# Kernel optimization log

Hardware: AMD Instinct MI355X
Metric: run time of the kernel (lower is better)

The kernel has to match this reference:

```python
import jax, jax.numpy as jnp
import numpy as np

N = 2708       # hardcoded in the original forward (Cora)
INS = 1433
OUTS = 64
M = 8          # N_mechs
HID = 64       # conditioner hidden width
LEAK = 0.2
NEG = -1e9


def setup_inputs() -> dict:
    key = jax.random.key(0)
    ks = jax.random.split(key, 9)
    x = jax.random.normal(ks[0], (N, INS), dtype=jnp.float32)
    adj = jax.random.randint(ks[1], (N, N), 0, 2) > 0  # bool mask
    adj = adj | jnp.eye(N, dtype=bool)                 # ensure self-loops so softmax is well-defined
    s = 1.0 / np.sqrt(INS)
    W = jax.random.normal(ks[2], (M, INS, OUTS), dtype=jnp.float32) * s
    a_src = jax.random.normal(ks[3], (M, OUTS), dtype=jnp.float32) * (1.0 / np.sqrt(OUTS))
    a_dst = jax.random.normal(ks[4], (M, OUTS), dtype=jnp.float32) * (1.0 / np.sqrt(OUTS))
    Wc1 = jax.random.normal(ks[5], (INS, HID), dtype=jnp.float32) * s
    bc1 = jnp.zeros((HID,), dtype=jnp.float32)
    Wc2 = jax.random.normal(ks[6], (HID, 2 * M), dtype=jnp.float32) * (1.0 / np.sqrt(HID))
    bc2 = jnp.zeros((2 * M,), dtype=jnp.float32)
    return {"x": x, "adj": adj, "W": W, "a_src": a_src, "a_dst": a_dst,
            "Wc1": Wc1, "bc1": bc1, "Wc2": Wc2, "bc2": bc2}


def reference(x, adj, W, a_src, a_dst, Wc1, bc1, Wc2, bc2):
    # dropout is identity in eval mode.
    # Conditioner MLP applied per node (vectorized over the Python loop in the original):
    cond = jax.nn.relu(x @ Wc1 + bc1) @ Wc2 + bc2          # [N, 2M]
    c = cond.reshape(N, 2, M)                               # matches cond.view(2708, 2, -1)
    gamma = c[:, 0, :].T                                    # [M, N] per-node scalar gamma per mechanism
    beta = c[:, 1, :].T                                     # [M, N]
    # All mechanisms batched: project + FiLM modulate
    h = jnp.einsum('nf,mfo->mno', x, W)                     # [M, N, OUTS]
    h = gamma[:, :, None] * h + beta[:, :, None]
    # GAT scoring: e_ij = LeakyReLU(a_src.h_i + a_dst.h_j), masked by adj
    e_src = jnp.einsum('mno,mo->mn', h, a_src)              # [M, N]
    e_dst = jnp.einsum('mno,mo->mn', h, a_dst)              # [M, N]
    e = jax.nn.leaky_relu(e_src[:, :, None] + e_dst[:, None, :], LEAK)  # [M, N, N]
    e = jnp.where(adj[None, :, :], e, NEG)
    attn = jax.nn.softmax(e, axis=-1)                       # [M, N, N]
    out = jnp.einsum('mnk,mko->mno', attn, h)               # [M, N, OUTS]
    # concat=True: cat over mechanisms along feature dim
    out = jnp.transpose(out, (1, 0, 2)).reshape(N, M * OUTS)  # [N, M*OUTS]
    return out
```

## Files before the change

### kernel.cpp

```cpp
#include <hip/hip_runtime.h>

#define NN   2708
#define INS  1433
#define MM   8
#define NP   2720
#define WPR  85
#define KP   1440
#define NKC  45
#define RP   2752
#define C9   576
#define OC   512

#define CAN_ASRC 0
#define CAN_ADST 512
#define CAN_BC1  1024
#define CAN_BC2  1088
#define CAN_WC2  1104
#define CAN_TOT  2128

#define ADJ_WAVES (NN * 11)
#define ADJBLK ((ADJ_WAVES + 3) / 4)
#define XBLK   1935
#define WTBLK  (9 * 23)
#define PACK_TOT (ADJBLK + XBLK + WTBLK + 1)

typedef unsigned short u16;
typedef unsigned int   u32;
typedef __attribute__((ext_vector_type(8))) short bf16x8;
typedef __attribute__((ext_vector_type(4))) float f32x4;

static __device__ __forceinline__ u16 f2bfu(float f) {
    union { float f; u32 u; } v; v.f = f;
    u32 u = v.u;
    u32 r = (u + 0x7fffu + ((u >> 16) & 1u)) >> 16;
    return (u16)r;
}
static __device__ __forceinline__ float bfu2f(u16 b) {
    union { u32 u; float f; } v; v.u = ((u32)b) << 16;
    return v.f;
}

static __device__ __forceinline__ int xfp32_of(const int* ctr) {
    int s = 0;
    #pragma unroll
    for (int k = 0; k < 32; ++k) s += ctr[k];
    return s > 32;
}
static __device__ __forceinline__ int aflag_decode(int b) {
    if (b & 2)  return 3;
    if (b & 4)  return 4;
    if (b & 8)  return 5;
    if (b & 1)  return 1;
    if (b & 16) return 0;
    return 2;
}

__global__ void k_probe(const u32* __restrict__ x_raw, const u32* __restrict__ adj_raw,
                        int* __restrict__ ctr) {
    const int b = blockIdx.x, t = threadIdx.x;
    __shared__ int sred[4];
    if (b < 32) {
        int local = 0;
        #pragma unroll
        for (int k = 0; k < 8; ++k) {
            u32 v = x_raw[b * 2048 + k * 256 + t];
            u32 lo = v & 0xffffu, hi = v >> 16;
            if ((lo & 0x7f80u) == 0u && lo != 0u) local++;
            if ((hi & 0x7f80u) == 0u && hi != 0u) local++;
        }
        #pragma unroll
        for (int off = 32; off > 0; off >>= 1) local += __shfl_xor(local, off, 64);
        if ((t & 63) == 0) sred[t >> 6] = local;
        __syncthreads();
        if (t == 0) ctr[b] = sred[0] + sred[1] + sred[2] + sred[3];
    } else {
        int fl = 0;
        #pragma unroll
        for (int k = 0; k < 8; ++k) {
            int w = (b - 32) * 2048 + k * 256 + t;
            u32 v = adj_raw[w];
            if (v > 1u)           fl |= 1;
            if (v == 0x3f803f80u) fl |= 2;
            if (v == 0x3f800000u) fl |= 4;
            if (v == 0x3c003c00u) fl |= 8;
            if ((w & 1) && v)     fl |= 16;
        }
        #pragma unroll
        for (int off = 32; off > 0; off >>= 1) fl |= __shfl_xor(fl, off, 64);
        if ((t & 63) == 0) sred[t >> 6] = fl;
        __syncthreads();
        if (t == 0) ctr[b] = sred[0] | sred[1] | sred[2] | sred[3];
    }
}

static __device__ __forceinline__ u16 load_as_bf16(const void* p, size_t idx, int fp32) {
    if (fp32) return f2bfu(((const float*)p)[idx]);
    return ((const u16*)p)[idx];
}
static __device__ __forceinline__ float load_as_f32(const void* p, size_t idx, int fp32) {
    if (fp32) return ((const float*)p)[idx];
    return bfu2f(((const u16*)p)[idx]);
}

__global__ void k_pack(const void* __restrict__ x, const void* __restrict__ adj,
                       const void* __restrict__ W, const void* __restrict__ Wc1,
                       const void* a_src, const void* a_dst, const void* bc1,
                       const void* bc2, const void* Wc2,
                       u16* __restrict__ xpf, u16* __restrict__ WTf,
                       u32* __restrict__ adjT, float* __restrict__ canon,
                       const int* __restrict__ ctr) {
    __shared__ float lds[64][65];
    __shared__ int sflags[2];
    const int t = threadIdx.x;
    if (t < 64) {
        int v = ctr[t];
        int cnt  = (t < 32) ? v : 0;
        int bits = (t >= 32) ? v : 0;
        #pragma unroll
        for (int off = 32; off > 0; off >>= 1) {
            cnt  += __shfl_xor(cnt, off, 64);
            bits |= __shfl_xor(bits, off, 64);
        }
        if (t == 0) { sflags[0] = cnt; sflags[1] = bits; }
    }
    __syncthreads();
    const int fp32 = sflags[0] > 32;

    const int bid = blockIdx.x;
    if (bid < ADJBLK) {
        const int f = aflag_decode(sflags[1]);
        const int wid  = bid * 4 + (t >> 6);
        const int lane = t & 63;
        const int i = wid / 11;
        const int c256 = wid - i * 11;
        if (i >= NN) return;
        const int jb0 = c256 * 256;
        #pragma unroll
        for (int s = 0; s < 4; ++s) {
            const int jb = jb0 + s * 64;
            if (jb >= NP) break;
            const int j = jb + lane;
            int v = 0;
            if (j < NN) {
                size_t idx = (size_t)i * NN + j;
                if      (f == 0) v = ((const int*)adj)[idx] != 0;
                else if (f == 1) v = ((const unsigned char*)adj)[idx] != 0;
                else if (f == 2) v = ((const long long*)adj)[idx] != 0;
                else if (f == 4) v = ((const float*)adj)[idx] != 0.f;
                else             v = ((const u16*)adj)[idx] != 0;
            }
            unsigned long long mask = __ballot(v);
            if (lane == 0) {
                const int ww = jb >> 5;
                adjT[(size_t)ww * NP + i] = (u32)mask;
                if (ww + 1 < WPR) adjT[(size_t)(ww + 1) * NP + i] = (u32)(mask >> 32);
            }
        }
    } else if (bid < ADJBLK + XBLK) {
        const int base = (bid - ADJBLK) * 2048 + t;
        #pragma unroll
        for (int s = 0; s < 8; ++s) {
            const int e = base + s * 256;
            const int t1 = e >> 9, sub = e & 511;
            const int r = sub >> 5, kloc = sub & 31;
            const int it = t1 / NKC, kc = t1 - it * NKC;
            const int row = it * 16 + r, col = kc * 32 + kloc;
            u16 v = 0;
            if (row < NN && col < INS) v = load_as_bf16(x, (size_t)row * INS + col, fp32);
            xpf[e] = v;
        }
    } else if (bid < ADJBLK + XBLK + WTBLK) {
        const int b2 = bid - ADJBLK - XBLK;
        const int mblk = b2 / 23, ktile = b2 - mblk * 23;
        #pragma unroll
        for (int ii = 0; ii < 16; ++ii) {
            int l = t * 16 + ii;
            int k_in = l >> 6, o = l & 63;
            int k = ktile * 64 + k_in;
            float v = 0.f;
            if (k < INS) {
                if (mblk < 8) v = load_as_f32(W, ((size_t)mblk * INS + k) * 64 + o, fp32);
                else          v = load_as_f32(Wc1, (size_t)k * 64 + o, fp32);
            }
            lds[k_in][o] = v;
        }
        __syncthreads();
        #pragma unroll
        for (int ii = 0; ii < 16; ++ii) {
            int e2 = t * 16 + ii;
            int ct2 = e2 >> 10, kc2 = (e2 >> 9) & 1;
            int r = (e2 >> 5) & 15, kloc = e2 & 31;
            int kc = ktile * 2 + kc2;
            if (kc < NKC) {
                int ct = mblk * 4 + ct2;
                WTf[(((size_t)ct * NKC + kc) * 16 + r) * 32 + kloc] =
                    f2bfu(lds[kc2 * 32 + kloc][ct2 * 16 + r]);
            }
        }
    } else {
        for (int e = t; e < CAN_TOT; e += 256) {
            float v;
            if      (e < CAN_ADST) v = load_as_f32(a_src, e - CAN_ASRC, fp32);
            else if (e < CAN_BC1)  v = load_as_f32(a_dst, e - CAN_ADST, fp32);
            else if (e < CAN_BC2)  v = load_as_f32(bc1,  e - CAN_BC1, fp32);
            else if (e < CAN_WC2)  v = load_as_f32(bc2,  e - CAN_BC2, fp32);
            else                   v = load_as_f32(Wc2,  e - CAN_WC2, fp32);
            canon[e] = v;
        }
    }
}

__launch_bounds__(64)
__global__ void k_gemm(const u16* __restrict__ xpf, const u16* __restrict__ WTf,
                       float* __restrict__ h_pre) {
    const int lane = threadIdx.x;
    const int r    = lane & 15;
    const int quad = lane >> 4;
    const int it0  = blockIdx.x * 2;
    const int ct0  = blockIdx.y * 2;

    const u16* aP0 = xpf + (size_t)it0 * NKC * 512 + r * 32 + quad * 8;
    const u16* aP1 = aP0 + (size_t)NKC * 512;
    const u16* bP0 = WTf + (size_t)ct0 * NKC * 512 + r * 32 + quad * 8;
    const u16* bP1 = bP0 + (size_t)NKC * 512;

    f32x4 acc[2][2];
    #pragma unroll
    for (int a = 0; a < 2; ++a)
        #pragma unroll
        for (int b = 0; b < 2; ++b) acc[a][b] = (f32x4){0.f, 0.f, 0.f, 0.f};

    #pragma unroll 3
    for (int kc = 0; kc < NKC; ++kc) {
        bf16x8 a0 = *(const bf16x8*)(aP0 + kc * 512);
        bf16x8 a1 = *(const bf16x8*)(aP1 + kc * 512);
        bf16x8 b0 = *(const bf16x8*)(bP0 + kc * 512);
        bf16x8 b1 = *(const bf16x8*)(bP1 + kc * 512);
        acc[0][0] = __builtin_amdgcn_mfma_f32_16x16x32_bf16(a0, b0, acc[0][0], 0, 0, 0);
        acc[0][1] = __builtin_amdgcn_mfma_f32_16x16x32_bf16(a0, b1, acc[0][1], 0, 0, 0);
        acc[1][0] = __builtin_amdgcn_mfma_f32_16x16x32_bf16(a1, b0, acc[1][0], 0, 0, 0);
        acc[1][1] = __builtin_amdgcn_mfma_f32_16x16x32_bf16(a1, b1, acc[1][1], 0, 0, 0);
    }

    #pragma unroll
    for (int a = 0; a < 2; ++a) {
        #pragma unroll
        for (int reg = 0; reg < 4; ++reg) {
            const int ii = (it0 + a) * 16 + quad * 4 + reg;
            if (ii < NN) {
                float* orow = h_pre + (size_t)ii * C9 + ct0 * 16;
                orow[ 0 + r] = acc[a][0][reg];
                orow[16 + r] = acc[a][1][reg];
            }
        }
    }
}

__launch_bounds__(256)
__global__ void k_film(const float* __restrict__ h_pre, const float* __restrict__ canon,
                       u16* __restrict__ HTf, float* __restrict__ e_srcP,
                       float* __restrict__ e_dstP) {
    const int m  = blockIdx.y;
    const int n0 = blockIdx.x * 32;
    const int t  = threadIdx.x, wave = t >> 6, o = t & 63;
    __shared__ u16 hbuf[32][66];

    const float wg = canon[CAN_WC2 + o * 16 + m];
    const float wb = canon[CAN_WC2 + o * 16 + m + 8];
    const float as = canon[CAN_ASRC + m * 64 + o];
    const float ad = canon[CAN_ADST + m * 64 + o];
    const float b1 = canon[CAN_BC1 + o];
    const float g0 = canon[CAN_BC2 + m], b0 = canon[CAN_BC2 + m + 8];

    #pragma unroll
    for (int it = 0; it < 8; ++it) {
        const int nl = wave * 8 + it, n = n0 + nl;
        const bool valid = n < NN;
        float hv = 0.f;
        if (valid) hv = h_pre[(size_t)n * C9 + 512 + o] + b1;
        hv = hv > 0.f ? hv : 0.f;
        float pg = hv * wg, pb = hv * wb;
        #pragma unroll
        for (int off = 32; off > 0; off >>= 1) {
            pg += __shfl_xor(pg, off, 64);
            pb += __shfl_xor(pb, off, 64);
        }
        const float g = pg + g0, bb = pb + b0;
        float h = 0.f;
        if (valid) h = g * h_pre[(size_t)n * C9 + m * 64 + o] + bb;
        float ps = h * as, pd = h * ad;
        #pragma unroll
        for (int off = 32; off > 0; off >>= 1) {
            ps += __shfl_xor(ps, off, 64);
            pd += __shfl_xor(pd, off, 64);
        }
        if (o == 0) { e_srcP[m * NP + n] = ps; e_dstP[m * NP + n] = pd; }
        hbuf[nl][o] = f2bfu(h);
    }
    __syncthreads();
    u32* ht32 = (u32*)(HTf + ((size_t)m * WPR + (n0 >> 5)) * 2048);
    #pragma unroll
    for (int rep = 0; rep < 4; ++rep) {
        const int idx = rep * 256 + t;
        const int oo = idx >> 4, jp = idx & 15;
        ht32[idx] = (u32)hbuf[2 * jp][oo] | ((u32)hbuf[2 * jp + 1][oo] << 16);
    }
}

__global__ void k_prep(const float* __restrict__ e_srcP, const float* __restrict__ e_dstP,
                       float* __restrict__ E1P, float* __restrict__ E2P,
                       float* __restrict__ F1P, float* __restrict__ F2P) {
    const int m = blockIdx.x, sl = blockIdx.y, t = threadIdx.x;
    const float* ed = e_dstP + m * NP;
    const float* es = e_srcP + m * NP;
    float mx = -3.0e38f;
    for (int j = t; j < NP; j += 256) mx = fmaxf(mx, ed[j]);
    #pragma unroll
    for (int off = 32; off > 0; off >>= 1) mx = fmaxf(mx, __shfl_xor(mx, off, 64));
    __shared__ float sm[4];
    if ((t & 63) == 0) sm[t >> 6] = mx;
    __syncthreads();
    const float maxd = fmaxf(fmaxf(sm[0], sm[1]), fmaxf(sm[2], sm[3]));
    const int j0 = sl * (NP / 8);
    for (int j = j0 + t; j < j0 + NP / 8; j += 256) {
        const float d = ed[j] - maxd;
        E1P[m * NP + j] = __expf(d);
        E2P[m * NP + j] = __expf(0.2f * d);
    }
    for (int i = j0 + t; i < j0 + NP / 8; i += 256) {
        const float v = es[i] + maxd;
        const float rmax = v > 0.f ? v : 0.2f * v;
        F1P[m * NP + i] = __expf(v - rmax);
        F2P[m * NP + i] = __expf(0.2f * v - rmax);
    }
}

__launch_bounds__(256)
__global__ void k_attn(const u32* __restrict__ adjT, const float* __restrict__ F1P,
                       const float* __restrict__ F2P, const float* __restrict__ E1P,
                       const float* __restrict__ E2P, const u16* __restrict__ HTf,
                       void* __restrict__ outv, const int* __restrict__ ctr) {
    const int m = blockIdx.y, i0 = blockIdx.x * 16;
    const int t = threadIdx.x;
    const int wave = t >> 6, lane = t & 63;
    const int r = lane & 15, quad = lane >> 4;
    const int i = min(i0 + r, NN - 1);

    __shared__ float sE[2 * NP];
    __shared__ u32 sAdj[WPR * 16];

    for (int idx = t; idx < NP; idx += 256) {
        sE[idx]      = E1P[m * NP + idx];
        sE[NP + idx] = E2P[m * NP + idx];
    }
    for (int w = t; w < WPR * 16; w += 256) {
        const int tile = w >> 4, rr = w & 15;
        sAdj[w] = adjT[(size_t)tile * NP + min(i0 + rr, NN - 1)];
    }
    __syncthreads();

    const float F1 = F1P[m * NP + i], F2 = F2P[m * NP + i];
    const u16* hbase = HTf + (size_t)m * WPR * 2048 + r * 32 + quad * 8;

    f32x4 acc[4], accl;
    #pragma unroll
    for (int nt = 0; nt < 4; ++nt) acc[nt] = (f32x4){0.f, 0.f, 0.f, 0.f};
    accl = (f32x4){0.f, 0.f, 0.f, 0.f};

    bf16x8 ones;
    #pragma unroll
    for (int kk = 0; kk < 8; ++kk) ones[kk] = (short)0x3f80;

    #pragma unroll 2
    for (int jc = wave * 32; jc < NP; jc += 128) {
        const int jb = jc + quad * 8;
        const int tile = jc >> 5;
        const float4 a0 = *(const float4*)(sE + jb);
        const float4 a1 = *(const float4*)(sE + jb + 4);
        const float4 b0 = *(const float4*)(sE + NP + jb);
        const float4 b1 = *(const float4*)(sE + NP + jb + 4);
        const u32 w = sAdj[tile * 16 + r];
        const u32 mask8 = (w >> (quad * 8)) & 0xffu;
        float p[8];
        p[0] = fmaxf(F1 * a0.x, F2 * b0.x);
        p[1] = fmaxf(F1 * a0.y, F2 * b0.y);
        p[2] = fmaxf(F1 * a0.z, F2 * b0.z);
        p[3] = fmaxf(F1 * a0.w, F2 * b0.w);
        p[4] = fmaxf(F1 * a1.x, F2 * b1.x);
        p[5] = fmaxf(F1 * a1.y, F2 * b1.y);
        p[6] = fmaxf(F1 * a1.z, F2 * b1.z);
        p[7] = fmaxf(F1 * a1.w, F2 * b1.w);
        bf16x8 af;
        #pragma unroll
        for (int kk = 0; kk < 8; ++kk) {
            const float pv = ((mask8 >> kk) & 1u) ? p[kk] : 0.f;
            af[kk] = (short)f2bfu(pv);
        }
        const u16* ht = hbase + (size_t)tile * 2048;
        #pragma unroll
        for (int nt = 0; nt < 4; ++nt) {
            bf16x8 bf = *(const bf16x8*)(ht + nt * 512);
            acc[nt] = __builtin_amdgcn_mfma_f32_16x16x32_bf16(af, bf, acc[nt], 0, 0, 0);
        }
        accl = __builtin_amdgcn_mfma_f32_16x16x32_bf16(af, ones, accl, 0, 0, 0);
    }

    __syncthreads();
    float* red = sE;
    #pragma unroll
    for (int nt = 0; nt < 4; ++nt)
        #pragma unroll
        for (int reg = 0; reg < 4; ++reg)
            red[(wave * 64 + lane) * 21 + nt * 4 + reg] = acc[nt][reg];
    #pragma unroll
    for (int reg = 0; reg < 4; ++reg)
        red[(wave * 64 + lane) * 21 + 16 + reg] = accl[reg];
    __syncthreads();
    if (wave != 0) return;

    #pragma unroll
    for (int nt = 0; nt < 4; ++nt)
        #pragma unroll
        for (int reg = 0; reg < 4; ++reg)
            acc[nt][reg] = red[lane * 21 + nt * 4 + reg] + red[(64 + lane) * 21 + nt * 4 + reg]
                         + red[(128 + lane) * 21 + nt * 4 + reg] + red[(192 + lane) * 21 + nt * 4 + reg];
    #pragma unroll
    for (int reg = 0; reg < 4; ++reg)
        accl[reg] = red[lane * 21 + 16 + reg] + red[(64 + lane) * 21 + 16 + reg]
                  + red[(128 + lane) * 21 + 16 + reg] + red[(192 + lane) * 21 + 16 + reg];

    const int ofp32 = xfp32_of(ctr);
    #pragma unroll
    for (int reg = 0; reg < 4; ++reg) {
        const int ii = i0 + quad * 4 + reg;
        if (ii < NN) {
            const float lr = accl[reg];
            const float inv = (lr > 0.f) ? 1.f / lr : 0.f;
            #pragma unroll
            for (int nt = 0; nt < 4; ++nt) {
                const float o = acc[nt][reg] * inv;
                const size_t idx = (size_t)ii * OC + m * 64 + nt * 16 + r;
                if (ofp32) ((float*)outv)[idx] = o;
                else       ((u16*)outv)[idx]   = f2bfu(o);
            }
        }
    }
}

extern "C" void kernel_launch(void* const* d_in, const int* in_sizes, int n_in,
                              void* d_out, int out_size, void* d_ws, size_t ws_size,
                              hipStream_t stream) {
    (void)in_sizes; (void)n_in; (void)out_size; (void)ws_size;
    const void* x     = d_in[0];
    const void* adj   = d_in[1];
    const void* W     = d_in[2];
    const void* a_src = d_in[3];
    const void* a_dst = d_in[4];
    const void* Wc1   = d_in[5];
    const void* bc1   = d_in[6];
    const void* Wc2   = d_in[7];
    const void* bc2   = d_in[8];

    char* ws = (char*)d_ws;
    size_t off = 0;
    auto alloc = [&](size_t bytes) -> void* {
        void* p = ws + off;
        off += (bytes + 255) & ~(size_t)255;
        return p;
    };
    u16*   xpf     = (u16*)  alloc((size_t)RP * KP * 2);
    u16*   WTf     = (u16*)  alloc((size_t)C9 * KP * 2);
    float* h_pre   = (float*)alloc((size_t)NN * C9 * 4);
    float* e_srcP  = (float*)alloc((size_t)MM * NP * 4);
    float* e_dstP  = (float*)alloc((size_t)MM * NP * 4);
    float* E1P     = (float*)alloc((size_t)MM * NP * 4);
    float* E2P     = (float*)alloc((size_t)MM * NP * 4);
    float* F1P     = (float*)alloc((size_t)MM * NP * 4);
    float* F2P     = (float*)alloc((size_t)MM * NP * 4);
    u16*   HTf     = (u16*)  alloc((size_t)MM * WPR * 2048 * 2);
    u32*   adjT    = (u32*)  alloc((size_t)WPR * NP * 4);
    float* canon   = (float*)alloc((size_t)CAN_TOT * 4);
    int*   ctr     = (int*)  alloc(256);

    hipLaunchKernelGGL(k_probe, dim3(64), dim3(256), 0, stream,
                       (const u32*)x, (const u32*)adj, ctr);
    hipLaunchKernelGGL(k_pack, dim3(PACK_TOT), dim3(256), 0, stream,
                       x, adj, W, Wc1, a_src, a_dst, bc1, bc2, Wc2,
                       xpf, WTf, adjT, canon, ctr);
    hipLaunchKernelGGL(k_gemm, dim3(RP / 32, 18), dim3(64), 0, stream, xpf, WTf, h_pre);
    hipLaunchKernelGGL(k_film, dim3(NP / 32, MM), dim3(256), 0, stream,
                       h_pre, canon, HTf, e_srcP, e_dstP);
    hipLaunchKernelGGL(k_prep, dim3(MM, 8), dim3(256), 0, stream,
                       e_srcP, e_dstP, E1P, E2P, F1P, F2P);
    hipLaunchKernelGGL(k_attn, dim3((NN + 15) / 16, MM), dim3(256), 0, stream,
                       adjT, F1P, F2P, E1P, E2P, HTf, d_out, ctr);
}
```

Measured before the change: 196.9 us.

## Fuse softmax prep into film and attention kernels via atomic max

Removes the separate k_prep kernel. The per-mechanism e_dst max is now computed in k_film with an order-preserving uint atomicMax. The exp factors are recomputed inside k_attn while it stages to LDS. bf16 packing switches to packed hardware conversion intrinsics, and the output dtype flag is computed once per block into shared memory. This saves a launch and intermediate global arrays, at the cost of redundant exp work in every attention block. It also relies on atomic initialization in k_pack, and padded rows beyond NN in k_film may feed zero values into the max.

```diff
diff --git a/kernel.cpp b/kernel.cpp
--- a/kernel.cpp
+++ b/kernel.cpp
@@ -1,4 +1,5 @@
 #include <hip/hip_runtime.h>
+#include <hip/hip_bf16.h>
 
 #define NN   2708
 #define INS  1433
@@ -39,13 +40,20 @@
     union { u32 u; float f; } v; v.u = ((u32)b) << 16;
     return v.f;
 }
-
-static __device__ __forceinline__ int xfp32_of(const int* ctr) {
-    int s = 0;
-    #pragma unroll
-    for (int k = 0; k < 32; ++k) s += ctr[k];
-    return s > 32;
-}
+static __device__ __forceinline__ u32 pk_bf16(float a, float b) {
+    union { __hip_bfloat162 h; u32 w; } p;
+    p.h = __float22bfloat162_rn(make_float2(a, b));
+    return p.w;
+}
+static __device__ __forceinline__ u32 fkey(float f) {
+    u32 u = __float_as_uint(f);
+    return (u & 0x80000000u) ? ~u : (u | 0x80000000u);
+}
+static __device__ __forceinline__ float funkey(u32 k) {
+    u32 u = (k & 0x80000000u) ? (k & 0x7fffffffu) : ~k;
+    return __uint_as_float(u);
+}
+
 static __device__ __forceinline__ int aflag_decode(int b) {
     if (b & 2)  return 3;
     if (b & 4)  return 4;
@@ -108,7 +116,7 @@
                        const void* bc2, const void* Wc2,
                        u16* __restrict__ xpf, u16* __restrict__ WTf,
                        u32* __restrict__ adjT, float* __restrict__ canon,
-                       const int* __restrict__ ctr) {
+                       u32* __restrict__ maxdKey, const int* __restrict__ ctr) {
     __shared__ float lds[64][65];
     __shared__ int sflags[2];
     const int t = threadIdx.x;
@@ -198,6 +206,7 @@
             }
         }
     } else {
+        if (t < 8) maxdKey[t] = 0u;
         for (int e = t; e < CAN_TOT; e += 256) {
             float v;
             if      (e < CAN_ADST) v = load_as_f32(a_src, e - CAN_ASRC, fp32);
@@ -259,11 +268,12 @@
 __launch_bounds__(256)
 __global__ void k_film(const float* __restrict__ h_pre, const float* __restrict__ canon,
                        u16* __restrict__ HTf, float* __restrict__ e_srcP,
-                       float* __restrict__ e_dstP) {
+                       float* __restrict__ e_dstP, u32* __restrict__ maxdKey) {
     const int m  = blockIdx.y;
     const int n0 = blockIdx.x * 32;
     const int t  = threadIdx.x, wave = t >> 6, o = t & 63;
-    __shared__ u16 hbuf[32][66];
+    __shared__ float hbuf[32][66];
+    __shared__ float smx[4];
 
     const float wg = canon[CAN_WC2 + o * 16 + m];
     const float wb = canon[CAN_WC2 + o * 16 + m + 8];
@@ -272,6 +282,7 @@
     const float b1 = canon[CAN_BC1 + o];
     const float g0 = canon[CAN_BC2 + m], b0 = canon[CAN_BC2 + m + 8];
 
+    float mxd = -3.0e38f;
     #pragma unroll
     for (int it = 0; it < 8; ++it) {
         const int nl = wave * 8 + it, n = n0 + nl;
@@ -295,51 +306,29 @@
             pd += __shfl_xor(pd, off, 64);
         }
         if (o == 0) { e_srcP[m * NP + n] = ps; e_dstP[m * NP + n] = pd; }
-        hbuf[nl][o] = f2bfu(h);
-    }
+        mxd = fmaxf(mxd, pd);
+        hbuf[nl][o] = h;
+    }
+    if (o == 0) smx[wave] = mxd;
     __syncthreads();
+    if (t == 0) {
+        const float bm = fmaxf(fmaxf(smx[0], smx[1]), fmaxf(smx[2], smx[3]));
+        atomicMax(&maxdKey[m], fkey(bm));
+    }
     u32* ht32 = (u32*)(HTf + ((size_t)m * WPR + (n0 >> 5)) * 2048);
     #pragma unroll
     for (int rep = 0; rep < 4; ++rep) {
         const int idx = rep * 256 + t;
         const int oo = idx >> 4, jp = idx & 15;
-        ht32[idx] = (u32)hbuf[2 * jp][oo] | ((u32)hbuf[2 * jp + 1][oo] << 16);
-    }
-}
-
-__global__ void k_prep(const float* __restrict__ e_srcP, const float* __restrict__ e_dstP,
-                       float* __restrict__ E1P, float* __restrict__ E2P,
-                       float* __restrict__ F1P, float* __restrict__ F2P) {
-    const int m = blockIdx.x, sl = blockIdx.y, t = threadIdx.x;
-    const float* ed = e_dstP + m * NP;
-    const float* es = e_srcP + m * NP;
-    float mx = -3.0e38f;
-    for (int j = t; j < NP; j += 256) mx = fmaxf(mx, ed[j]);
-    #pragma unroll
-    for (int off = 32; off > 0; off >>= 1) mx = fmaxf(mx, __shfl_xor(mx, off, 64));
-    __shared__ float sm[4];
-    if ((t & 63) == 0) sm[t >> 6] = mx;
-    __syncthreads();
-    const float maxd = fmaxf(fmaxf(sm[0], sm[1]), fmaxf(sm[2], sm[3]));
-    const int j0 = sl * (NP / 8);
-    for (int j = j0 + t; j < j0 + NP / 8; j += 256) {
-        const float d = ed[j] - maxd;
-        E1P[m * NP + j] = __expf(d);
-        E2P[m * NP + j] = __expf(0.2f * d);
-    }
-    for (int i = j0 + t; i < j0 + NP / 8; i += 256) {
-        const float v = es[i] + maxd;
-        const float rmax = v > 0.f ? v : 0.2f * v;
-        F1P[m * NP + i] = __expf(v - rmax);
-        F2P[m * NP + i] = __expf(0.2f * v - rmax);
+        ht32[idx] = pk_bf16(hbuf[2 * jp][oo], hbuf[2 * jp + 1][oo]);
     }
 }
 
 __launch_bounds__(256)
-__global__ void k_attn(const u32* __restrict__ adjT, const float* __restrict__ F1P,
-                       const float* __restrict__ F2P, const float* __restrict__ E1P,
-                       const float* __restrict__ E2P, const u16* __restrict__ HTf,
-                       void* __restrict__ outv, const int* __restrict__ ctr) {
+__global__ void k_attn(const u32* __restrict__ adjT, const float* __restrict__ e_srcP,
+                       const float* __restrict__ e_dstP, const u32* __restrict__ maxdKey,
+                       const u16* __restrict__ HTf, void* __restrict__ outv,
+                       const int* __restrict__ ctr) {
     const int m = blockIdx.y, i0 = blockIdx.x * 16;
     const int t = threadIdx.x;
     const int wave = t >> 6, lane = t & 63;
@@ -348,10 +337,19 @@
 
     __shared__ float sE[2 * NP];
     __shared__ u32 sAdj[WPR * 16];
-
+    __shared__ int sflag;
+
+    const float maxd = funkey(maxdKey[m]);
+    if (t == 0) {
+        int s = 0;
+        #pragma unroll
+        for (int k = 0; k < 32; ++k) s += ctr[k];
+        sflag = s > 32;
+    }
     for (int idx = t; idx < NP; idx += 256) {
-        sE[idx]      = E1P[m * NP + idx];
-        sE[NP + idx] = E2P[m * NP + idx];
+        const float d = e_dstP[m * NP + idx] - maxd;
+        sE[idx]      = __expf(d);
+        sE[NP + idx] = __expf(0.2f * d);
     }
     for (int w = t; w < WPR * 16; w += 256) {
         const int tile = w >> 4, rr = w & 15;
@@ -359,7 +357,10 @@
     }
     __syncthreads();
 
-    const float F1 = F1P[m * NP + i], F2 = F2P[m * NP + i];
+    const float v0 = e_srcP[m * NP + i] + maxd;
+    const float rmax = v0 > 0.f ? v0 : 0.2f * v0;
+    const float F1 = __expf(v0 - rmax);
+    const float F2 = __expf(0.2f * v0 - rmax);
     const u16* hbase = HTf + (size_t)m * WPR * 2048 + r * 32 + quad * 8;
 
     f32x4 acc[4], accl;
@@ -390,19 +391,21 @@
         p[5] = fmaxf(F1 * a1.y, F2 * b1.y);
         p[6] = fmaxf(F1 * a1.z, F2 * b1.z);
         p[7] = fmaxf(F1 * a1.w, F2 * b1.w);
-        bf16x8 af;
-        #pragma unroll
-        for (int kk = 0; kk < 8; ++kk) {
-            const float pv = ((mask8 >> kk) & 1u) ? p[kk] : 0.f;
-            af[kk] = (short)f2bfu(pv);
-        }
+        #pragma unroll
+        for (int kk = 0; kk < 8; ++kk)
+            p[kk] = ((mask8 >> kk) & 1u) ? p[kk] : 0.f;
+        union { bf16x8 v; u32 w4[4]; } af;
+        af.w4[0] = pk_bf16(p[0], p[1]);
+        af.w4[1] = pk_bf16(p[2], p[3]);
+        af.w4[2] = pk_bf16(p[4], p[5]);
+        af.w4[3] = pk_bf16(p[6], p[7]);
         const u16* ht = hbase + (size_t)tile * 2048;
         #pragma unroll
         for (int nt = 0; nt < 4; ++nt) {
             bf16x8 bf = *(const bf16x8*)(ht + nt * 512);
-            acc[nt] = __builtin_amdgcn_mfma_f32_16x16x32_bf16(af, bf, acc[nt], 0, 0, 0);
-        }
-        accl = __builtin_amdgcn_mfma_f32_16x16x32_bf16(af, ones, accl, 0, 0, 0);
+            acc[nt] = __builtin_amdgcn_mfma_f32_16x16x32_bf16(af.v, bf, acc[nt], 0, 0, 0);
+        }
+        accl = __builtin_amdgcn_mfma_f32_16x16x32_bf16(af.v, ones, accl, 0, 0, 0);
     }
 
     __syncthreads();
@@ -429,7 +432,7 @@
         accl[reg] = red[lane * 21 + 16 + reg] + red[(64 + lane) * 21 + 16 + reg]
                   + red[(128 + lane) * 21 + 16 + reg] + red[(192 + lane) * 21 + 16 + reg];
 
-    const int ofp32 = xfp32_of(ctr);
+    const int ofp32 = sflag;
     #pragma unroll
     for (int reg = 0; reg < 4; ++reg) {
         const int ii = i0 + quad * 4 + reg;
@@ -473,25 +476,20 @@
     float* h_pre   = (float*)alloc((size_t)NN * C9 * 4);
     float* e_srcP  = (float*)alloc((size_t)MM * NP * 4);
     float* e_dstP  = (float*)alloc((size_t)MM * NP * 4);
-    float* E1P     = (float*)alloc((size_t)MM * NP * 4);
-    float* E2P     = (float*)alloc((size_t)MM * NP * 4);
-    float* F1P     = (float*)alloc((size_t)MM * NP * 4);
-    float* F2P     = (float*)alloc((size_t)MM * NP * 4);
     u16*   HTf     = (u16*)  alloc((size_t)MM * WPR * 2048 * 2);
     u32*   adjT    = (u32*)  alloc((size_t)WPR * NP * 4);
     float* canon   = (float*)alloc((size_t)CAN_TOT * 4);
+    u32*   maxdKey = (u32*)  alloc(256);
     int*   ctr     = (int*)  alloc(256);
 
     hipLaunchKernelGGL(k_probe, dim3(64), dim3(256), 0, stream,
                        (const u32*)x, (const u32*)adj, ctr);
     hipLaunchKernelGGL(k_pack, dim3(PACK_TOT), dim3(256), 0, stream,
                        x, adj, W, Wc1, a_src, a_dst, bc1, bc2, Wc2,
-                       xpf, WTf, adjT, canon, ctr);
+                       xpf, WTf, adjT, canon, maxdKey, ctr);
     hipLaunchKernelGGL(k_gemm, dim3(RP / 32, 18), dim3(64), 0, stream, xpf, WTf, h_pre);
     hipLaunchKernelGGL(k_film, dim3(NP / 32, MM), dim3(256), 0, stream,
-                       h_pre, canon, HTf, e_srcP, e_dstP);
-    hipLaunchKernelGGL(k_prep, dim3(MM, 8), dim3(256), 0, stream,
-                       e_srcP, e_dstP, E1P, E2P, F1P, F2P);
+                       h_pre, canon, HTf, e_srcP, e_dstP, maxdKey);
     hipLaunchKernelGGL(k_attn, dim3((NN + 15) / 16, MM), dim3(256), 0, stream,
-                       adjT, F1P, F2P, E1P, E2P, HTf, d_out, ctr);
-}
+                       adjT, e_srcP, e_dstP, maxdKey, HTf, d_out, ctr);
+}
```

Result: no change. 196.7 us, median of 2 (-0.1%).
